# Optimization experiments

Hardware: AMD Instinct MI355X
Metric: run time of the kernel (lower is better)

Reference implementation:

```python
import jax, jax.numpy as jnp
import numpy as np

N_NODES = 100000
N_EDGES = 1600000
IN_FEATS = 128
H1, H2 = 100, 200
OUT_FEATS = 64


def _glorot(key, shape):
    fan_in, fan_out = shape
    limit = float(np.sqrt(6.0 / (fan_in + fan_out)))
    return jax.random.uniform(key, shape, jnp.float32, -limit, limit)


def setup_inputs() -> dict:
    key = jax.random.key(0)
    ks = jax.random.split(key, 9)
    x = jax.random.normal(ks[0], (N_NODES, IN_FEATS), jnp.float32)
    edge_src = jax.random.randint(ks[1], (N_EDGES,), 0, N_NODES, jnp.int32)
    edge_dst = jax.random.randint(ks[2], (N_EDGES,), 0, N_NODES, jnp.int32)
    W1 = _glorot(ks[3], (IN_FEATS, H1)); b1 = jnp.zeros((H1,), jnp.float32)
    W2 = _glorot(ks[4], (H1, H2));       b2 = jnp.zeros((H2,), jnp.float32)
    W3 = _glorot(ks[5], (H2, OUT_FEATS)); b3 = jnp.zeros((OUT_FEATS,), jnp.float32)
    return {"x": x, "edge_src": edge_src, "edge_dst": edge_dst,
            "W1": W1, "b1": b1, "W2": W2, "b2": b2, "W3": W3, "b3": b3}


def _gcn_layer(h, src, dst, norm_src, norm_dst, W, b):
    # DGL GraphConv, norm='both': D_out^{-1/2} applied at src, sum-aggregate,
    # D_in^{-1/2} at dst, then dense linear + bias.
    h = h * norm_src[:, None]
    msgs = h[src]                                   # [E, d] gather
    agg = jax.ops.segment_sum(msgs, dst, num_segments=N_NODES)  # scatter-add
    agg = agg * norm_dst[:, None]
    return agg @ W + b


def reference(x, edge_src, edge_dst, W1, b1, W2, b2, W3, b3):
    ones = jnp.ones((N_EDGES,), jnp.float32)
    deg_out = jax.ops.segment_sum(ones, edge_src, num_segments=N_NODES)
    deg_in = jax.ops.segment_sum(ones, edge_dst, num_segments=N_NODES)
    norm_src = jax.lax.rsqrt(jnp.maximum(deg_out, 1.0))
    norm_dst = jax.lax.rsqrt(jnp.maximum(deg_in, 1.0))

    h = _gcn_layer(x, edge_src, edge_dst, norm_src, norm_dst, W1, b1)
    h = jax.nn.elu(h)
    h = _gcn_layer(h, edge_src, edge_dst, norm_src, norm_dst, W2, b2)
    h = jax.nn.elu(h)
    h = _gcn_layer(h, edge_src, edge_dst, norm_src, norm_dst, W3, b3)
    return jax.nn.sigmoid(h)
```

## Files before the change

kernel.cpp:

```cpp
#include <hip/hip_runtime.h>
#include <hip/hip_bf16.h>
#include <math.h>

#define NN 100000
#define NE 1600000

#define NBUCK 8
#define BSZ (NN / NBUCK)
#define CHUNKS 64
#define CH_E (NE / CHUNKS)
#define FILL_BLOCKS (NBUCK * CHUNKS)
#define GEMM_GRID ((NN / 16 + 3) / 4)

#define SCAN_BLK 256
#define NB_SCAN ((NN + SCAN_BLK - 1) / SCAN_BLK)

typedef float f32x4 __attribute__((ext_vector_type(4)));
typedef short s16x8 __attribute__((ext_vector_type(8)));
typedef unsigned short u16x4 __attribute__((ext_vector_type(4)));
typedef int i32x4 __attribute__((ext_vector_type(4)));

static inline int grid_for(long total, int block, long cap = 16384) {
    long b = (total + block - 1) / block;
    if (b > cap) b = cap;
    if (b < 1) b = 1;
    return (int)b;
}

__device__ __forceinline__ unsigned short f2b(float f) {
    __hip_bfloat16 h = __float2bfloat16(f);
    return __builtin_bit_cast(unsigned short, h);
}
__device__ __forceinline__ float b2f(unsigned short u) {
    unsigned int x = ((unsigned int)u) << 16;
    return __builtin_bit_cast(float, x);
}


__global__ __launch_bounds__(256) void partial_hist_kernel(
    const int* __restrict__ src, const int* __restrict__ dst,
    int* __restrict__ scratch)
{
    __shared__ int h[BSZ];
    int g = blockIdx.x & 7, c = blockIdx.x >> 3;
    int lo = g * BSZ;
    for (int i = threadIdx.x; i < BSZ; i += 256) h[i] = 0;
    __syncthreads();
    const i32x4* src4 = reinterpret_cast<const i32x4*>(src + c * CH_E);
    const i32x4* dst4 = reinterpret_cast<const i32x4*>(dst + c * CH_E);
    for (int i = threadIdx.x; i < CH_E / 4; i += 256) {
        i32x4 s4 = src4[i];
        i32x4 d4 = dst4[i];
#pragma unroll
        for (int j = 0; j < 4; ++j) {
            unsigned si = (unsigned)(s4[j] - lo);
            unsigned di = (unsigned)(d4[j] - lo);
            if (si < BSZ) atomicAdd(&h[si], 1);
            if (di < BSZ) atomicAdd(&h[di], 0x10000);
        }
    }
    __syncthreads();
    int* o = scratch + ((size_t)g * CHUNKS + c) * BSZ;
    for (int i = threadIdx.x; i < BSZ; i += 256) o[i] = h[i];
}

__global__ void reduce_hist_kernel(const int* __restrict__ scratch,
                                   float* __restrict__ ns, float* __restrict__ nd,
                                   int* __restrict__ cnt_dst) {
    int n = blockIdx.x * blockDim.x + threadIdx.x;
    if (n >= NN) return;
    int g = n / BSZ, i = n - g * BSZ;
    const int* p = scratch + (size_t)g * CHUNKS * BSZ + i;
    unsigned cs = 0, cd = 0;
#pragma unroll 8
    for (int c = 0; c < CHUNKS; ++c) {
        unsigned v = (unsigned)p[(size_t)c * BSZ];
        cs += v & 0xffffu;
        cd += v >> 16;
    }
    ns[n] = rsqrtf(fmaxf((float)cs, 1.0f));
    nd[n] = rsqrtf(fmaxf((float)cd, 1.0f));
    cnt_dst[n] = (int)cd;
}

__global__ void block_sum_kernel(const int* __restrict__ cnt, int* __restrict__ partials) {
    __shared__ int sm[SCAN_BLK];
    int i = blockIdx.x * SCAN_BLK + threadIdx.x;
    sm[threadIdx.x] = (i < NN) ? cnt[i] : 0;
    __syncthreads();
    for (int s = SCAN_BLK / 2; s > 0; s >>= 1) {
        if (threadIdx.x < s) sm[threadIdx.x] += sm[threadIdx.x + s];
        __syncthreads();
    }
    if (threadIdx.x == 0) partials[blockIdx.x] = sm[0];
}

__global__ void scan_partials_kernel(int* __restrict__ p) {
    __shared__ int sm[512];
    int tid = threadIdx.x;
    int v = (tid < NB_SCAN) ? p[tid] : 0;
    sm[tid] = v;
    __syncthreads();
    for (int off = 1; off < 512; off <<= 1) {
        int t = (tid >= off) ? sm[tid - off] : 0;
        __syncthreads();
        sm[tid] += t;
        __syncthreads();
    }
    if (tid < NB_SCAN) p[tid] = sm[tid] - v;
}

__global__ void block_scan_kernel(const int* __restrict__ cnt, const int* __restrict__ partials,
                                  int* __restrict__ row_ptr) {
    __shared__ int sm[SCAN_BLK];
    int i = blockIdx.x * SCAN_BLK + threadIdx.x;
    int v = (i < NN) ? cnt[i] : 0;
    sm[threadIdx.x] = v;
    __syncthreads();
    for (int off = 1; off < SCAN_BLK; off <<= 1) {
        int t = (threadIdx.x >= off) ? sm[threadIdx.x - off] : 0;
        __syncthreads();
        sm[threadIdx.x] += t;
        __syncthreads();
    }
    if (i < NN) {
        int excl = partials[blockIdx.x] + sm[threadIdx.x] - v;
        row_ptr[i] = excl;
        if (i == NN - 1) row_ptr[NN] = excl + v;
    }
}

__global__ void chunk_offs_kernel(int* __restrict__ scratch, const int* __restrict__ row_ptr) {
    int n = blockIdx.x * blockDim.x + threadIdx.x;
    if (n >= NN) return;
    int g = n / BSZ, i = n - g * BSZ;
    int* pd = scratch + (size_t)g * CHUNKS * BSZ + i;
    int base = row_ptr[n];
#pragma unroll 8
    for (int c = 0; c < CHUNKS; ++c) {
        unsigned cnt = ((unsigned)pd[(size_t)c * BSZ]) >> 16;
        pd[(size_t)c * BSZ] = base;
        base += (int)cnt;
    }
}


template <int K_REAL, int N_REAL, int NTILES>
__device__ __forceinline__ void repack_one(const float* __restrict__ W,
                                           unsigned short* __restrict__ Wf, int t) {
    int j = t & 7, lane = (t >> 3) & 63, frag = t >> 9;
    int kt = frag / NTILES, nt = frag - kt * NTILES;
    int k = kt * 32 + (lane >> 4) * 8 + j;
    int n = nt * 16 + (lane & 15);
    float v = (k < K_REAL && n < N_REAL) ? W[(size_t)k * N_REAL + n] : 0.0f;
    Wf[t] = f2b(v);
}

#define R1_N (28 * 512)
#define R2_N (56 * 512)
#define R3_N (28 * 512)

__global__ void prep_kernel(const float* __restrict__ W1, unsigned short* __restrict__ W1f,
                            const float* __restrict__ W2, unsigned short* __restrict__ W2f,
                            const float* __restrict__ W3, unsigned short* __restrict__ W3f,
                            const float* __restrict__ b2, float* __restrict__ b2p) {
    int t = blockIdx.x * blockDim.x + threadIdx.x;
    if (t < R1_N) {
        repack_one<128, 100, 7>(W1, W1f, t);
    } else if (t < R1_N + R2_N) {
        repack_one<100, 200, 14>(W2, W2f, t - R1_N);
    } else if (t < R1_N + R2_N + R3_N) {
        repack_one<200, 64, 4>(W3, W3f, t - R1_N - R2_N);
    } else if (t < R1_N + R2_N + R3_N + 224) {
        int i = t - R1_N - R2_N - R3_N;
        b2p[i] = (i < 200) ? b2[i] : 0.0f;
    }
}

template <int K_STEPS, int NTILES, int N_REAL, int EPI, int K_PAD, int AMODE>
__device__ __forceinline__ void gemm_body(
    int wave, int lane, const void* __restrict__ Aptr,
    const unsigned short* __restrict__ Wf, const float* __restrict__ rowscale,
    const float* __restrict__ bias, void* __restrict__ outv)
{
    int row0 = wave << 4;
    if (row0 >= NN) return;
    int r = lane & 15, half = lane >> 4;

    f32x4 acc[NTILES];
#pragma unroll
    for (int nt = 0; nt < NTILES; ++nt) acc[nt] = (f32x4)(0.0f);

#pragma unroll
    for (int kt = 0; kt < K_STEPS; ++kt) {
        s16x8 a;
        if (AMODE == 0) {
            const unsigned short* arow = (const unsigned short*)Aptr
                + (size_t)(row0 + r) * K_PAD + half * 8 + kt * 32;
            a = *reinterpret_cast<const s16x8*>(arow);
        } else {
            const float* arow = (const float*)Aptr
                + (size_t)(row0 + r) * K_PAD + half * 8 + kt * 32;
            f32x4 alo = *reinterpret_cast<const f32x4*>(arow);
            f32x4 ahi = *reinterpret_cast<const f32x4*>(arow + 4);
#pragma unroll
            for (int j = 0; j < 4; ++j) {
                a[j]     = (short)f2b(alo[j]);
                a[4 + j] = (short)f2b(ahi[j]);
            }
        }
#pragma unroll
        for (int nt = 0; nt < NTILES; ++nt) {
            s16x8 b = *reinterpret_cast<const s16x8*>(
                Wf + (((kt * NTILES + nt) << 9) | (lane << 3)));
            acc[nt] = __builtin_amdgcn_mfma_f32_16x16x32_bf16(a, b, acc[nt], 0, 0, 0);
        }
    }

    int colbase = lane & 15;
    float rs[4];
#pragma unroll
    for (int j = 0; j < 4; ++j) rs[j] = rowscale[row0 + half * 4 + j];

    if (EPI == 2) {
        unsigned short* out = (unsigned short*)outv;
#pragma unroll
        for (int nt = 0; nt < NTILES; ++nt) {
            int col = nt * 16 + colbase;
            if (col < N_REAL) {
#pragma unroll
                for (int j = 0; j < 4; ++j) {
                    int row = row0 + half * 4 + j;
                    out[(size_t)row * N_REAL + col] = f2b(acc[nt][j] * rs[j]);
                }
            }
        }
    } else {
        unsigned short* out = (unsigned short*)outv;
        const int NOUT = NTILES * 16;
#pragma unroll
        for (int nt = 0; nt < NTILES; ++nt) {
            int col = nt * 16 + colbase;
            float bv = bias[col];
#pragma unroll
            for (int j = 0; j < 4; ++j) {
                int row = row0 + half * 4 + j;
                float v = acc[nt][j] * rs[j] + bv;
                v = (v > 0.0f) ? v : expm1f(v);
                out[(size_t)row * NOUT + col] = f2b(v);
            }
        }
    }
}

template <int K_STEPS, int NTILES, int N_REAL, int EPI, int K_PAD, int AMODE>
__global__ __launch_bounds__(256) void gemm_kernel(
    const void* __restrict__ Aptr, const unsigned short* __restrict__ Wf,
    const float* __restrict__ rowscale, const float* __restrict__ bias,
    void* __restrict__ outv)
{
    int wave = blockIdx.x * (blockDim.x >> 6) + (threadIdx.x >> 6);
    gemm_body<K_STEPS, NTILES, N_REAL, EPI, K_PAD, AMODE>(
        wave, threadIdx.x & 63, Aptr, Wf, rowscale, bias, outv);
}

__global__ __launch_bounds__(256) void fill_gemm1_kernel(
    const int* __restrict__ src, const int* __restrict__ dst,
    const int* __restrict__ scratch, int* __restrict__ col_src,
    const float* __restrict__ x, const unsigned short* __restrict__ W1f,
    const float* __restrict__ ns, unsigned short* __restrict__ y1)
{
    __shared__ int off[BSZ];
    if (blockIdx.x < FILL_BLOCKS) {
        int g = blockIdx.x & 7, c = blockIdx.x >> 3;
        int lo = g * BSZ;
        const int* pd = scratch + ((size_t)g * CHUNKS + c) * BSZ;
        for (int i = threadIdx.x; i < BSZ; i += 256) off[i] = pd[i];
        __syncthreads();
        const i32x4* src4 = reinterpret_cast<const i32x4*>(src + c * CH_E);
        const i32x4* dst4 = reinterpret_cast<const i32x4*>(dst + c * CH_E);
        for (int i = threadIdx.x; i < CH_E / 4; i += 256) {
            i32x4 s4 = src4[i];
            i32x4 d4 = dst4[i];
#pragma unroll
            for (int j = 0; j < 4; ++j) {
                unsigned di = (unsigned)(d4[j] - lo);
                if (di < BSZ) {
                    int p = atomicAdd(&off[di], 1);
                    col_src[p] = s4[j];
                }
            }
        }
    } else {
        int bid = blockIdx.x - FILL_BLOCKS;
        int wave = bid * 4 + (threadIdx.x >> 6);
        gemm_body<4, 7, 100, 2, 128, 1>(wave, threadIdx.x & 63, x, W1f, ns, nullptr, y1);
    }
}


#define GACC8(yb, stride)                                                        \
    int i = start;                                                               \
    f32x4 a0 = (f32x4)(0.0f), a1 = (f32x4)(0.0f), a2 = (f32x4)(0.0f),            \
          a3 = (f32x4)(0.0f);                                                    \
    for (; i + 8 <= end; i += 8) {                                               \
        int s0 = col_src[i],     s1 = col_src[i + 1];                            \
        int s2 = col_src[i + 2], s3 = col_src[i + 3];                            \
        int s4 = col_src[i + 4], s5 = col_src[i + 5];                            \
        int s6 = col_src[i + 6], s7 = col_src[i + 7];                            \
        u16x4 v0 = *reinterpret_cast<const u16x4*>(yb + (size_t)s0 * stride + g * 4); \
        u16x4 v1 = *reinterpret_cast<const u16x4*>(yb + (size_t)s1 * stride + g * 4); \
        u16x4 v2 = *reinterpret_cast<const u16x4*>(yb + (size_t)s2 * stride + g * 4); \
        u16x4 v3 = *reinterpret_cast<const u16x4*>(yb + (size_t)s3 * stride + g * 4); \
        u16x4 v4 = *reinterpret_cast<const u16x4*>(yb + (size_t)s4 * stride + g * 4); \
        u16x4 v5 = *reinterpret_cast<const u16x4*>(yb + (size_t)s5 * stride + g * 4); \
        u16x4 v6 = *reinterpret_cast<const u16x4*>(yb + (size_t)s6 * stride + g * 4); \
        u16x4 v7 = *reinterpret_cast<const u16x4*>(yb + (size_t)s7 * stride + g * 4); \
        _Pragma("unroll")                                                        \
        for (int j = 0; j < 4; ++j) {                                            \
            a0[j] += b2f(v0[j]) + b2f(v4[j]);                                    \
            a1[j] += b2f(v1[j]) + b2f(v5[j]);                                    \
            a2[j] += b2f(v2[j]) + b2f(v6[j]);                                    \
            a3[j] += b2f(v3[j]) + b2f(v7[j]);                                    \
        }                                                                        \
    }                                                                            \
    for (; i + 4 <= end; i += 4) {                                               \
        int s0 = col_src[i], s1 = col_src[i + 1];                                \
        int s2 = col_src[i + 2], s3 = col_src[i + 3];                            \
        u16x4 v0 = *reinterpret_cast<const u16x4*>(yb + (size_t)s0 * stride + g * 4); \
        u16x4 v1 = *reinterpret_cast<const u16x4*>(yb + (size_t)s1 * stride + g * 4); \
        u16x4 v2 = *reinterpret_cast<const u16x4*>(yb + (size_t)s2 * stride + g * 4); \
        u16x4 v3 = *reinterpret_cast<const u16x4*>(yb + (size_t)s3 * stride + g * 4); \
        _Pragma("unroll")                                                        \
        for (int j = 0; j < 4; ++j) {                                            \
            a0[j] += b2f(v0[j]); a1[j] += b2f(v1[j]);                            \
            a2[j] += b2f(v2[j]); a3[j] += b2f(v3[j]);                            \
        }                                                                        \
    }                                                                            \
    for (; i < end; ++i) {                                                       \
        int s0 = col_src[i];                                                     \
        u16x4 v0 = *reinterpret_cast<const u16x4*>(yb + (size_t)s0 * stride + g * 4); \
        _Pragma("unroll")                                                        \
        for (int j = 0; j < 4; ++j) a0[j] += b2f(v0[j]);                         \
    }                                                                            \
    f32x4 acc;                                                                   \
    _Pragma("unroll")                                                            \
    for (int j = 0; j < 4; ++j) acc[j] = (a0[j] + a1[j]) + (a2[j] + a3[j]);

__global__ void gather1_kernel(const unsigned short* __restrict__ y, const int* __restrict__ row_ptr,
                               const int* __restrict__ col_src, const float* __restrict__ ns,
                               const float* __restrict__ nd, const float* __restrict__ bias,
                               unsigned short* __restrict__ out) {
    unsigned t = blockIdx.x * blockDim.x + threadIdx.x;
    if (t >= NN * 25u) return;
    unsigned n = t / 25u, g = t - n * 25u;
    int start = row_ptr[n], end = row_ptr[n + 1];
    GACC8(y, 100)
    f32x4 b4 = *reinterpret_cast<const f32x4*>(bias + g * 4);
    float ndv = nd[n], nsv = ns[n];
    u16x4 o;
#pragma unroll
    for (int j = 0; j < 4; ++j) {
        float v = acc[j] * ndv + b4[j];
        v = (v > 0.0f) ? v : expm1f(v);
        o[j] = f2b(v * nsv);
    }
    *reinterpret_cast<u16x4*>(out + (size_t)n * 100 + g * 4) = o;
}

__global__ void gather2_kernel(const unsigned short* __restrict__ y, const int* __restrict__ row_ptr,
                               const int* __restrict__ col_src, unsigned short* __restrict__ out) {
    unsigned t = blockIdx.x * blockDim.x + threadIdx.x;
    if (t >= NN * 32u) return;
    unsigned n = t >> 5, g = t & 31u;
    if (g >= 25u) {
        u16x4 z = (u16x4)(0);
        *reinterpret_cast<u16x4*>(out + (size_t)n * 128 + 100 + (g - 25u) * 4) = z;
        return;
    }
    int start = row_ptr[n], end = row_ptr[n + 1];
    GACC8(y, 100)
    u16x4 o;
#pragma unroll
    for (int j = 0; j < 4; ++j) o[j] = f2b(acc[j]);
    *reinterpret_cast<u16x4*>(out + (size_t)n * 128 + g * 4) = o;
}

__global__ void gather3_kernel(const unsigned short* __restrict__ y, const int* __restrict__ row_ptr,
                               const int* __restrict__ col_src, const float* __restrict__ nd,
                               const float* __restrict__ bias, float* __restrict__ out) {
    unsigned t = blockIdx.x * blockDim.x + threadIdx.x;
    if (t >= NN * 16u) return;
    unsigned n = t >> 4, g = t & 15u;
    int start = row_ptr[n], end = row_ptr[n + 1];
    GACC8(y, 64)
    f32x4 b4 = *reinterpret_cast<const f32x4*>(bias + g * 4);
    float ndv = nd[n];
    f32x4 o;
#pragma unroll
    for (int j = 0; j < 4; ++j) {
        float v = acc[j] * ndv + b4[j];
        o[j] = 1.0f / (1.0f + expf(-v));
    }
    *reinterpret_cast<f32x4*>(out + (size_t)n * 64 + g * 4) = o;
}


extern "C" void kernel_launch(void* const* d_in, const int* in_sizes, int n_in,
                              void* d_out, int out_size, void* d_ws, size_t ws_size,
                              hipStream_t stream) {
    const float* x    = (const float*)d_in[0];
    const int*   esrc = (const int*)d_in[1];
    const int*   edst = (const int*)d_in[2];
    const float* W1   = (const float*)d_in[3];
    const float* b1   = (const float*)d_in[4];
    const float* W2   = (const float*)d_in[5];
    const float* b2   = (const float*)d_in[6];
    const float* W3   = (const float*)d_in[7];
    const float* b3   = (const float*)d_in[8];
    float* out = (float*)d_out;

    char* base = (char*)d_ws;
    size_t off = 0;
    auto alloc = [&](size_t bytes) -> void* {
        void* p = base + off;
        off += (bytes + 255) & ~(size_t)255;
        return p;
    };
    void* region1 = alloc((size_t)NN * 128 * 2);
    void* region2 = alloc((size_t)NN * 224 * 2);
    void* region3 = alloc((size_t)NN * 100 * 2);
    float* ns       = (float*)alloc(NN * 4);
    float* nd       = (float*)alloc(NN * 4);
    int*   cnt_dst  = (int*)alloc(NN * 4);
    int*   row_ptr  = (int*)alloc((NN + 1) * 4);
    int*   col_src  = (int*)alloc((size_t)NE * 4);
    int*   partials = (int*)alloc(512 * 4);
    unsigned short* W1f = (unsigned short*)alloc(R1_N * 2);
    unsigned short* W2f = (unsigned short*)alloc(R2_N * 2);
    unsigned short* W3f = (unsigned short*)alloc(R3_N * 2);
    float* b2p = (float*)alloc(224 * 4);

    int* scratch          = (int*)region1;
    unsigned short* agg2b = (unsigned short*)region1;
    unsigned short* y3    = (unsigned short*)region1;
    unsigned short* y1    = (unsigned short*)region2;
    unsigned short* h2b   = (unsigned short*)region2;
    unsigned short* h1s   = (unsigned short*)region3;

    const int BLK = 256;

    prep_kernel<<<grid_for(R1_N + R2_N + R3_N + 224, BLK), BLK, 0, stream>>>(
        W1, W1f, W2, W2f, W3, W3f, b2, b2p);

    partial_hist_kernel<<<NBUCK * CHUNKS, 256, 0, stream>>>(esrc, edst, scratch);
    reduce_hist_kernel<<<grid_for(NN, BLK), BLK, 0, stream>>>(scratch, ns, nd, cnt_dst);
    block_sum_kernel<<<NB_SCAN, SCAN_BLK, 0, stream>>>(cnt_dst, partials);
    scan_partials_kernel<<<1, 512, 0, stream>>>(partials);
    block_scan_kernel<<<NB_SCAN, SCAN_BLK, 0, stream>>>(cnt_dst, partials, row_ptr);
    chunk_offs_kernel<<<grid_for(NN, BLK), BLK, 0, stream>>>(scratch, row_ptr);

    fill_gemm1_kernel<<<FILL_BLOCKS + GEMM_GRID, 256, 0, stream>>>(
        esrc, edst, scratch, col_src, x, W1f, ns, y1);

    gather1_kernel<<<grid_for((long)NN * 25, BLK, 1 << 30), BLK, 0, stream>>>(
        y1, row_ptr, col_src, ns, nd, b1, h1s);

    gather2_kernel<<<grid_for((long)NN * 32, BLK, 1 << 30), BLK, 0, stream>>>(
        h1s, row_ptr, col_src, agg2b);
    gemm_kernel<4, 14, 200, 1, 128, 0><<<GEMM_GRID, BLK, 0, stream>>>(agg2b, W2f, nd, b2p, h2b);

    gemm_kernel<7, 4, 64, 2, 224, 0><<<GEMM_GRID, BLK, 0, stream>>>(h2b, W3f, ns, nullptr, y3);
    gather3_kernel<<<grid_for((long)NN * 16, BLK, 1 << 30), BLK, 0, stream>>>(
        y3, row_ptr, col_src, nd, b3, out);
}
```

Measured before the change: 399.7 us.

## Fuse layer-2 gather into MFMA GEMM and merge preprocessing kernels

New measurement: 402.8 us. About the same (+0.8%).

```diff
diff --git a/kernel.cpp b/kernel.cpp
--- a/kernel.cpp
+++ b/kernel.cpp
@@ -15,9 +15,16 @@
 #define SCAN_BLK 256
 #define NB_SCAN ((NN + SCAN_BLK - 1) / SCAN_BLK)
 
+#define R1_N (28 * 512)
+#define R2_N (56 * 512)
+#define R3_N (28 * 512)
+#define PREP_TOTAL (R1_N + R2_N + R3_N + 224)
+#define PREP_BLOCKS ((PREP_TOTAL + 255) / 256)
+
 typedef float f32x4 __attribute__((ext_vector_type(4)));
 typedef short s16x8 __attribute__((ext_vector_type(8)));
 typedef unsigned short u16x4 __attribute__((ext_vector_type(4)));
+typedef unsigned short u16x8 __attribute__((ext_vector_type(8)));
 typedef int i32x4 __attribute__((ext_vector_type(4)));
 
 static inline int grid_for(long total, int block, long cap = 16384) {
@@ -36,12 +43,36 @@
     return __builtin_bit_cast(float, x);
 }
 
-
-__global__ __launch_bounds__(256) void partial_hist_kernel(
-    const int* __restrict__ src, const int* __restrict__ dst,
-    int* __restrict__ scratch)
+template <int K_REAL, int N_REAL, int NTILES>
+__device__ __forceinline__ void repack_one(const float* __restrict__ W,
+                                           unsigned short* __restrict__ Wf, int t) {
+    int j = t & 7, lane = (t >> 3) & 63, frag = t >> 9;
+    int kt = frag / NTILES, nt = frag - kt * NTILES;
+    int k = kt * 32 + (lane >> 4) * 8 + j;
+    int n = nt * 16 + (lane & 15);
+    float v = (k < K_REAL && n < N_REAL) ? W[(size_t)k * N_REAL + n] : 0.0f;
+    Wf[t] = f2b(v);
+}
+
+__global__ __launch_bounds__(256) void hist_prep_kernel(
+    const int* __restrict__ src, const int* __restrict__ dst, int* __restrict__ scratch,
+    const float* __restrict__ W1, unsigned short* __restrict__ W1f,
+    const float* __restrict__ W2, unsigned short* __restrict__ W2f,
+    const float* __restrict__ W3, unsigned short* __restrict__ W3f,
+    const float* __restrict__ b2, float* __restrict__ b2p)
 {
     __shared__ int h[BSZ];
+    if (blockIdx.x >= FILL_BLOCKS) {
+        int t = (blockIdx.x - FILL_BLOCKS) * 256 + threadIdx.x;
+        if (t < R1_N) repack_one<128, 100, 7>(W1, W1f, t);
+        else if (t < R1_N + R2_N) repack_one<100, 200, 14>(W2, W2f, t - R1_N);
+        else if (t < R1_N + R2_N + R3_N) repack_one<200, 64, 4>(W3, W3f, t - R1_N - R2_N);
+        else if (t < PREP_TOTAL) {
+            int i = t - R1_N - R2_N - R3_N;
+            b2p[i] = (i < 200) ? b2[i] : 0.0f;
+        }
+        return;
+    }
     int g = blockIdx.x & 7, c = blockIdx.x >> 3;
     int lo = g * BSZ;
     for (int i = threadIdx.x; i < BSZ; i += 256) h[i] = 0;
@@ -66,27 +97,26 @@
 
 __global__ void reduce_hist_kernel(const int* __restrict__ scratch,
                                    float* __restrict__ ns, float* __restrict__ nd,
-                                   int* __restrict__ cnt_dst) {
+                                   int* __restrict__ cnt_dst, int* __restrict__ partials) {
+    __shared__ int sm[SCAN_BLK];
     int n = blockIdx.x * blockDim.x + threadIdx.x;
-    if (n >= NN) return;
-    int g = n / BSZ, i = n - g * BSZ;
-    const int* p = scratch + (size_t)g * CHUNKS * BSZ + i;
-    unsigned cs = 0, cd = 0;
+    int cdv = 0;
+    if (n < NN) {
+        int g = n / BSZ, i = n - g * BSZ;
+        const int* p = scratch + (size_t)g * CHUNKS * BSZ + i;
+        unsigned cs = 0, cd = 0;
 #pragma unroll 8
-    for (int c = 0; c < CHUNKS; ++c) {
-        unsigned v = (unsigned)p[(size_t)c * BSZ];
-        cs += v & 0xffffu;
-        cd += v >> 16;
-    }
-    ns[n] = rsqrtf(fmaxf((float)cs, 1.0f));
-    nd[n] = rsqrtf(fmaxf((float)cd, 1.0f));
-    cnt_dst[n] = (int)cd;
-}
-
-__global__ void block_sum_kernel(const int* __restrict__ cnt, int* __restrict__ partials) {
-    __shared__ int sm[SCAN_BLK];
-    int i = blockIdx.x * SCAN_BLK + threadIdx.x;
-    sm[threadIdx.x] = (i < NN) ? cnt[i] : 0;
+        for (int c = 0; c < CHUNKS; ++c) {
+            unsigned v = (unsigned)p[(size_t)c * BSZ];
+            cs += v & 0xffffu;
+            cd += v >> 16;
+        }
+        ns[n] = rsqrtf(fmaxf((float)cs, 1.0f));
+        nd[n] = rsqrtf(fmaxf((float)cd, 1.0f));
+        cnt_dst[n] = (int)cd;
+        cdv = (int)cd;
+    }
+    sm[threadIdx.x] = cdv;
     __syncthreads();
     for (int s = SCAN_BLK / 2; s > 0; s >>= 1) {
         if (threadIdx.x < s) sm[threadIdx.x] += sm[threadIdx.x + s];
@@ -110,8 +140,8 @@
     if (tid < NB_SCAN) p[tid] = sm[tid] - v;
 }
 
-__global__ void block_scan_kernel(const int* __restrict__ cnt, const int* __restrict__ partials,
-                                  int* __restrict__ row_ptr) {
+__global__ void scan_offs_kernel(const int* __restrict__ cnt, const int* __restrict__ partials,
+                                 int* __restrict__ row_ptr, int* __restrict__ scratch) {
     __shared__ int sm[SCAN_BLK];
     int i = blockIdx.x * SCAN_BLK + threadIdx.x;
     int v = (i < NN) ? cnt[i] : 0;
@@ -127,61 +157,23 @@
         int excl = partials[blockIdx.x] + sm[threadIdx.x] - v;
         row_ptr[i] = excl;
         if (i == NN - 1) row_ptr[NN] = excl + v;
-    }
-}
-
-__global__ void chunk_offs_kernel(int* __restrict__ scratch, const int* __restrict__ row_ptr) {
-    int n = blockIdx.x * blockDim.x + threadIdx.x;
-    if (n >= NN) return;
-    int g = n / BSZ, i = n - g * BSZ;
-    int* pd = scratch + (size_t)g * CHUNKS * BSZ + i;
-    int base = row_ptr[n];
+        int g = i / BSZ, ii = i - g * BSZ;
+        int* pd = scratch + (size_t)g * CHUNKS * BSZ + ii;
+        int base = excl;
 #pragma unroll 8
-    for (int c = 0; c < CHUNKS; ++c) {
-        unsigned cnt = ((unsigned)pd[(size_t)c * BSZ]) >> 16;
-        pd[(size_t)c * BSZ] = base;
-        base += (int)cnt;
-    }
-}
-
-
-template <int K_REAL, int N_REAL, int NTILES>
-__device__ __forceinline__ void repack_one(const float* __restrict__ W,
-                                           unsigned short* __restrict__ Wf, int t) {
-    int j = t & 7, lane = (t >> 3) & 63, frag = t >> 9;
-    int kt = frag / NTILES, nt = frag - kt * NTILES;
-    int k = kt * 32 + (lane >> 4) * 8 + j;
-    int n = nt * 16 + (lane & 15);
-    float v = (k < K_REAL && n < N_REAL) ? W[(size_t)k * N_REAL + n] : 0.0f;
-    Wf[t] = f2b(v);
-}
-
-#define R1_N (28 * 512)
-#define R2_N (56 * 512)
-#define R3_N (28 * 512)
-
-__global__ void prep_kernel(const float* __restrict__ W1, unsigned short* __restrict__ W1f,
-                            const float* __restrict__ W2, unsigned short* __restrict__ W2f,
-                            const float* __restrict__ W3, unsigned short* __restrict__ W3f,
-                            const float* __restrict__ b2, float* __restrict__ b2p) {
-    int t = blockIdx.x * blockDim.x + threadIdx.x;
-    if (t < R1_N) {
-        repack_one<128, 100, 7>(W1, W1f, t);
-    } else if (t < R1_N + R2_N) {
-        repack_one<100, 200, 14>(W2, W2f, t - R1_N);
-    } else if (t < R1_N + R2_N + R3_N) {
-        repack_one<200, 64, 4>(W3, W3f, t - R1_N - R2_N);
-    } else if (t < R1_N + R2_N + R3_N + 224) {
-        int i = t - R1_N - R2_N - R3_N;
-        b2p[i] = (i < 200) ? b2[i] : 0.0f;
-    }
-}
-
-template <int K_STEPS, int NTILES, int N_REAL, int EPI, int K_PAD, int AMODE>
+        for (int c = 0; c < CHUNKS; ++c) {
+            unsigned cc = ((unsigned)pd[(size_t)c * BSZ]) >> 16;
+            pd[(size_t)c * BSZ] = base;
+            base += (int)cc;
+        }
+    }
+}
+
+template <int K_STEPS, int NTILES, int N_REAL, int K_PAD, int AMODE>
 __device__ __forceinline__ void gemm_body(
     int wave, int lane, const void* __restrict__ Aptr,
     const unsigned short* __restrict__ Wf, const float* __restrict__ rowscale,
-    const float* __restrict__ bias, void* __restrict__ outv)
+    void* __restrict__ outv)
 {
     int row0 = wave << 4;
     if (row0 >= NN) return;
@@ -222,46 +214,28 @@
 #pragma unroll
     for (int j = 0; j < 4; ++j) rs[j] = rowscale[row0 + half * 4 + j];
 
-    if (EPI == 2) {
-        unsigned short* out = (unsigned short*)outv;
-#pragma unroll
-        for (int nt = 0; nt < NTILES; ++nt) {
-            int col = nt * 16 + colbase;
-            if (col < N_REAL) {
-#pragma unroll
-                for (int j = 0; j < 4; ++j) {
-                    int row = row0 + half * 4 + j;
-                    out[(size_t)row * N_REAL + col] = f2b(acc[nt][j] * rs[j]);
-                }
-            }
-        }
-    } else {
-        unsigned short* out = (unsigned short*)outv;
-        const int NOUT = NTILES * 16;
-#pragma unroll
-        for (int nt = 0; nt < NTILES; ++nt) {
-            int col = nt * 16 + colbase;
-            float bv = bias[col];
+    unsigned short* out = (unsigned short*)outv;
+#pragma unroll
+    for (int nt = 0; nt < NTILES; ++nt) {
+        int col = nt * 16 + colbase;
+        if (col < N_REAL) {
 #pragma unroll
             for (int j = 0; j < 4; ++j) {
                 int row = row0 + half * 4 + j;
-                float v = acc[nt][j] * rs[j] + bv;
-                v = (v > 0.0f) ? v : expm1f(v);
-                out[(size_t)row * NOUT + col] = f2b(v);
+                out[(size_t)row * N_REAL + col] = f2b(acc[nt][j] * rs[j]);
             }
         }
     }
 }
 
-template <int K_STEPS, int NTILES, int N_REAL, int EPI, int K_PAD, int AMODE>
+template <int K_STEPS, int NTILES, int N_REAL, int K_PAD, int AMODE>
 __global__ __launch_bounds__(256) void gemm_kernel(
     const void* __restrict__ Aptr, const unsigned short* __restrict__ Wf,
-    const float* __restrict__ rowscale, const float* __restrict__ bias,
-    void* __restrict__ outv)
+    const float* __restrict__ rowscale, void* __restrict__ outv)
 {
     int wave = blockIdx.x * (blockDim.x >> 6) + (threadIdx.x >> 6);
-    gemm_body<K_STEPS, NTILES, N_REAL, EPI, K_PAD, AMODE>(
-        wave, threadIdx.x & 63, Aptr, Wf, rowscale, bias, outv);
+    gemm_body<K_STEPS, NTILES, N_REAL, K_PAD, AMODE>(
+        wave, threadIdx.x & 63, Aptr, Wf, rowscale, outv);
 }
 
 __global__ __launch_bounds__(256) void fill_gemm1_kernel(
@@ -294,7 +268,119 @@
     } else {
         int bid = blockIdx.x - FILL_BLOCKS;
         int wave = bid * 4 + (threadIdx.x >> 6);
-        gemm_body<4, 7, 100, 2, 128, 1>(wave, threadIdx.x & 63, x, W1f, ns, nullptr, y1);
+        gemm_body<4, 7, 100, 128, 1>(wave, threadIdx.x & 63, x, W1f, ns, y1);
+    }
+}
+
+__global__ __launch_bounds__(256) void gemm2_fused_kernel(
+    const unsigned short* __restrict__ h1s, const int* __restrict__ row_ptr,
+    const int* __restrict__ col_src, const unsigned short* __restrict__ Wf,
+    const float* __restrict__ nd, const float* __restrict__ b2p,
+    unsigned short* __restrict__ h2b)
+{
+    int wave = blockIdx.x * (blockDim.x >> 6) + (threadIdx.x >> 6);
+    int row0 = wave << 4;
+    if (row0 >= NN) return;
+    int lane = threadIdx.x & 63;
+    int r = lane & 15, half = lane >> 4;
+    int n = row0 + r;
+    int start = row_ptr[n], end = row_ptr[n + 1];
+
+    f32x4 g0a = (f32x4)(0.f), g0b = (f32x4)(0.f);
+    f32x4 g1a = (f32x4)(0.f), g1b = (f32x4)(0.f);
+    f32x4 g2a = (f32x4)(0.f), g2b = (f32x4)(0.f);
+    f32x4 g3a = (f32x4)(0.f);
+
+    int i = start;
+    for (; i + 2 <= end; i += 2) {
+        int s0 = col_src[i], s1 = col_src[i + 1];
+        const unsigned short* p0 = h1s + (size_t)s0 * 100 + half * 8;
+        const unsigned short* p1 = h1s + (size_t)s1 * 100 + half * 8;
+        u16x8 v00 = *reinterpret_cast<const u16x8*>(p0);
+        u16x8 v01 = *reinterpret_cast<const u16x8*>(p0 + 32);
+        u16x8 v02 = *reinterpret_cast<const u16x8*>(p0 + 64);
+        u16x8 v10 = *reinterpret_cast<const u16x8*>(p1);
+        u16x8 v11 = *reinterpret_cast<const u16x8*>(p1 + 32);
+        u16x8 v12 = *reinterpret_cast<const u16x8*>(p1 + 64);
+#pragma unroll
+        for (int j = 0; j < 4; ++j) {
+            g0a[j] += b2f(v00[j]) + b2f(v10[j]);
+            g0b[j] += b2f(v00[4 + j]) + b2f(v10[4 + j]);
+            g1a[j] += b2f(v01[j]) + b2f(v11[j]);
+            g1b[j] += b2f(v01[4 + j]) + b2f(v11[4 + j]);
+            g2a[j] += b2f(v02[j]) + b2f(v12[j]);
+            g2b[j] += b2f(v02[4 + j]) + b2f(v12[4 + j]);
+        }
+        if (half == 0) {
+            u16x4 w0 = *reinterpret_cast<const u16x4*>(p0 + 96);
+            u16x4 w1 = *reinterpret_cast<const u16x4*>(p1 + 96);
+#pragma unroll
+            for (int j = 0; j < 4; ++j) g3a[j] += b2f(w0[j]) + b2f(w1[j]);
+        }
+    }
+    for (; i < end; ++i) {
+        int s0 = col_src[i];
+        const unsigned short* p0 = h1s + (size_t)s0 * 100 + half * 8;
+        u16x8 v00 = *reinterpret_cast<const u16x8*>(p0);
+        u16x8 v01 = *reinterpret_cast<const u16x8*>(p0 + 32);
+        u16x8 v02 = *reinterpret_cast<const u16x8*>(p0 + 64);
+#pragma unroll
+        for (int j = 0; j < 4; ++j) {
+            g0a[j] += b2f(v00[j]);  g0b[j] += b2f(v00[4 + j]);
+            g1a[j] += b2f(v01[j]);  g1b[j] += b2f(v01[4 + j]);
+            g2a[j] += b2f(v02[j]);  g2b[j] += b2f(v02[4 + j]);
+        }
+        if (half == 0) {
+            u16x4 w0 = *reinterpret_cast<const u16x4*>(p0 + 96);
+#pragma unroll
+            for (int j = 0; j < 4; ++j) g3a[j] += b2f(w0[j]);
+        }
+    }
+
+    s16x8 a0, a1, a2, a3;
+#pragma unroll
+    for (int j = 0; j < 4; ++j) {
+        a0[j] = (short)f2b(g0a[j]);  a0[4 + j] = (short)f2b(g0b[j]);
+        a1[j] = (short)f2b(g1a[j]);  a1[4 + j] = (short)f2b(g1b[j]);
+        a2[j] = (short)f2b(g2a[j]);  a2[4 + j] = (short)f2b(g2b[j]);
+        a3[j] = (short)f2b(g3a[j]);  a3[4 + j] = 0;
+    }
+    if (half != 0) {
+#pragma unroll
+        for (int j = 0; j < 4; ++j) a3[j] = 0;
+    }
+
+    const int NTILES = 14;
+    f32x4 acc[NTILES];
+#pragma unroll
+    for (int nt = 0; nt < NTILES; ++nt) acc[nt] = (f32x4)(0.0f);
+#pragma unroll
+    for (int nt = 0; nt < NTILES; ++nt) {
+        s16x8 b0 = *reinterpret_cast<const s16x8*>(Wf + (((0 * NTILES + nt) << 9) | (lane << 3)));
+        s16x8 b1 = *reinterpret_cast<const s16x8*>(Wf + (((1 * NTILES + nt) << 9) | (lane << 3)));
+        s16x8 b2 = *reinterpret_cast<const s16x8*>(Wf + (((2 * NTILES + nt) << 9) | (lane << 3)));
+        s16x8 b3 = *reinterpret_cast<const s16x8*>(Wf + (((3 * NTILES + nt) << 9) | (lane << 3)));
+        acc[nt] = __builtin_amdgcn_mfma_f32_16x16x32_bf16(a0, b0, acc[nt], 0, 0, 0);
+        acc[nt] = __builtin_amdgcn_mfma_f32_16x16x32_bf16(a1, b1, acc[nt], 0, 0, 0);
+        acc[nt] = __builtin_amdgcn_mfma_f32_16x16x32_bf16(a2, b2, acc[nt], 0, 0, 0);
+        acc[nt] = __builtin_amdgcn_mfma_f32_16x16x32_bf16(a3, b3, acc[nt], 0, 0, 0);
+    }
+
+    int colbase = lane & 15;
+    float rs[4];
+#pragma unroll
+    for (int j = 0; j < 4; ++j) rs[j] = nd[row0 + half * 4 + j];
+#pragma unroll
+    for (int nt = 0; nt < NTILES; ++nt) {
+        int col = nt * 16 + colbase;
+        float bv = b2p[col];
+#pragma unroll
+        for (int j = 0; j < 4; ++j) {
+            int row = row0 + half * 4 + j;
+            float v = acc[nt][j] * rs[j] + bv;
+            v = (v > 0.0f) ? v : expm1f(v);
+            h2b[(size_t)row * 224 + col] = f2b(v);
+        }
     }
 }
 
@@ -368,24 +454,6 @@
     *reinterpret_cast<u16x4*>(out + (size_t)n * 100 + g * 4) = o;
 }
 
-__global__ void gather2_kernel(const unsigned short* __restrict__ y, const int* __restrict__ row_ptr,
-                               const int* __restrict__ col_src, unsigned short* __restrict__ out) {
-    unsigned t = blockIdx.x * blockDim.x + threadIdx.x;
-    if (t >= NN * 32u) return;
-    unsigned n = t >> 5, g = t & 31u;
-    if (g >= 25u) {
-        u16x4 z = (u16x4)(0);
-        *reinterpret_cast<u16x4*>(out + (size_t)n * 128 + 100 + (g - 25u) * 4) = z;
-        return;
-    }
-    int start = row_ptr[n], end = row_ptr[n + 1];
-    GACC8(y, 100)
-    u16x4 o;
-#pragma unroll
-    for (int j = 0; j < 4; ++j) o[j] = f2b(acc[j]);
-    *reinterpret_cast<u16x4*>(out + (size_t)n * 128 + g * 4) = o;
-}
-
 __global__ void gather3_kernel(const unsigned short* __restrict__ y, const int* __restrict__ row_ptr,
                                const int* __restrict__ col_src, const float* __restrict__ nd,
                                const float* __restrict__ bias, float* __restrict__ out) {
@@ -442,7 +510,6 @@
     float* b2p = (float*)alloc(224 * 4);
 
     int* scratch          = (int*)region1;
-    unsigned short* agg2b = (unsigned short*)region1;
     unsigned short* y3    = (unsigned short*)region1;
     unsigned short* y1    = (unsigned short*)region2;
     unsigned short* h2b   = (unsigned short*)region2;
@@ -450,15 +517,11 @@
 
     const int BLK = 256;
 
-    prep_kernel<<<grid_for(R1_N + R2_N + R3_N + 224, BLK), BLK, 0, stream>>>(
-        W1, W1f, W2, W2f, W3, W3f, b2, b2p);
-
-    partial_hist_kernel<<<NBUCK * CHUNKS, 256, 0, stream>>>(esrc, edst, scratch);
-    reduce_hist_kernel<<<grid_for(NN, BLK), BLK, 0, stream>>>(scratch, ns, nd, cnt_dst);
-    block_sum_kernel<<<NB_SCAN, SCAN_BLK, 0, stream>>>(cnt_dst, partials);
+    hist_prep_kernel<<<FILL_BLOCKS + PREP_BLOCKS, 256, 0, stream>>>(
+        esrc, edst, scratch, W1, W1f, W2, W2f, W3, W3f, b2, b2p);
+    reduce_hist_kernel<<<NB_SCAN, SCAN_BLK, 0, stream>>>(scratch, ns, nd, cnt_dst, partials);
     scan_partials_kernel<<<1, 512, 0, stream>>>(partials);
-    block_scan_kernel<<<NB_SCAN, SCAN_BLK, 0, stream>>>(cnt_dst, partials, row_ptr);
-    chunk_offs_kernel<<<grid_for(NN, BLK), BLK, 0, stream>>>(scratch, row_ptr);
+    scan_offs_kernel<<<NB_SCAN, SCAN_BLK, 0, stream>>>(cnt_dst, partials, row_ptr, scratch);
 
     fill_gemm1_kernel<<<FILL_BLOCKS + GEMM_GRID, 256, 0, stream>>>(
         esrc, edst, scratch, col_src, x, W1f, ns, y1);
@@ -466,11 +529,10 @@
     gather1_kernel<<<grid_for((long)NN * 25, BLK, 1 << 30), BLK, 0, stream>>>(
         y1, row_ptr, col_src, ns, nd, b1, h1s);
 
-    gather2_kernel<<<grid_for((long)NN * 32, BLK, 1 << 30), BLK, 0, stream>>>(
-        h1s, row_ptr, col_src, agg2b);
-    gemm_kernel<4, 14, 200, 1, 128, 0><<<GEMM_GRID, BLK, 0, stream>>>(agg2b, W2f, nd, b2p, h2b);
-
-    gemm_kernel<7, 4, 64, 2, 224, 0><<<GEMM_GRID, BLK, 0, stream>>>(h2b, W3f, ns, nullptr, y3);
+    gemm2_fused_kernel<<<GEMM_GRID, 256, 0, stream>>>(
+        h1s, row_ptr, col_src, W2f, nd, b2p, h2b);
+
+    gemm_kernel<7, 4, 64, 224, 0><<<GEMM_GRID, BLK, 0, stream>>>(h2b, W3f, ns, y3);
     gather3_kernel<<<grid_for((long)NN * 16, BLK, 1 << 30), BLK, 0, stream>>>(
         y3, row_ptr, col_src, nd, b3, out);
 }
```
